# Kernel tuning notes

Hardware: AMD Instinct MI355X
Metric: run time of the kernel (lower is better)

The kernel has to match this reference:

```python
import jax, jax.numpy as jnp
import numpy as np

B, C_IN, N = 4, 128, 4096
E = 131072           # nnz edges in the sparse adjacency
C_OUT = 128          # module out_channels
C_CONV = C_OUT - 1   # add_counts=True steals one channel for degree counts


def setup_inputs() -> dict:
    key = jax.random.key(0)
    kx, ki, kj, kw, kb = jax.random.split(key, 5)
    x = jax.random.normal(kx, (B, C_IN, N), dtype=jnp.float32)
    # edge list (i, j) for each nonzero of the sparse adjacency
    idx_i = jax.random.randint(ki, (E,), 0, N)
    idx_j = jax.random.randint(kj, (E,), 0, N)
    # Conv1d(in=C_IN, out=C_CONV, kernel_size=2, stride=2) weights
    W = jax.random.normal(kw, (C_CONV, C_IN, 2), dtype=jnp.float32) * 0.05
    b = jax.random.normal(kb, (C_CONV,), dtype=jnp.float32) * 0.05
    return {"x": x, "W": W, "b": b, "idx_i": idx_i, "idx_j": idx_j}


def reference(x, W, b, idx_i, idx_j):
    # _conv: x @ adj_pw.T is a gather of the two endpoints of every edge
    # (adj_pw row 2k selects node idx_i[k], row 2k+1 selects node idx_j[k]).
    # Conv1d(kernel=2, stride=2) then mixes the interleaved endpoint pair:
    #   pair[b,o,e] = sum_c W[o,c,0]*x[b,c,i_e] + W[o,c,1]*x[b,c,j_e] + b[o]
    xi = x[:, :, idx_i]                                   # [B, C, E]
    xj = x[:, :, idx_j]                                   # [B, C, E]
    pair = (jnp.einsum('oc,bce->boe', W[:, :, 0], xi)
            + jnp.einsum('oc,bce->boe', W[:, :, 1], xj)
            + b[None, :, None])                           # [B, C_CONV, E]
    # x @ adj_pw[::2, :] scatter-adds each edge's output to its first endpoint
    n = x.shape[2]
    y = jnp.zeros((x.shape[0], pair.shape[1], n), dtype=x.dtype)
    y = y.at[:, :, idx_i].add(pair)                       # [B, C_CONV, N]
    # adj_sum = adj.to_dense().sum(dim=0): in-degree over columns j
    deg = jnp.zeros((n,), dtype=x.dtype).at[idx_j].add(1.0)
    # normalize: divide by degree clamped to >= 1
    y = y / jnp.where(deg == 0, 1.0, deg)
    # add_counts: append raw degree as an extra channel
    counts = jnp.broadcast_to(deg[None, None, :], (y.shape[0], 1, n))
    return jnp.concatenate([y, counts], axis=1)           # [B, C_OUT, N]
```

## Files before the change

kernel.cpp:

```cpp
#include <hip/hip_runtime.h>
#include <cstdint>
#include <cstddef>

#define BATCH   4
#define CIN     128
#define NN      4096
#define EE      131072
#define CCONV   127
#define NBC     512
#define MAXDEG  128
#define CPAD    16

typedef __attribute__((ext_vector_type(8))) short short8;
typedef __attribute__((ext_vector_type(8))) unsigned short ushort8;
typedef __attribute__((ext_vector_type(4))) float f32x4;

__device__ __forceinline__ unsigned short f2bf(float f) {
    unsigned int u = __float_as_uint(f);
    return (unsigned short)((u + 0x7FFFu + ((u >> 16) & 1u)) >> 16);
}
__device__ __forceinline__ float bf2f(unsigned short h) {
    return __uint_as_float((unsigned int)h << 16);
}

__global__ __launch_bounds__(256) void k_pre(const float* __restrict__ x,
                                             unsigned short* __restrict__ xT,
                                             const float* __restrict__ W,
                                             unsigned short* __restrict__ WTb,
                                             const int* __restrict__ idx_i,
                                             const int* __restrict__ idx_j,
                                             int* __restrict__ cursor,
                                             unsigned short* __restrict__ elist,
                                             int* __restrict__ deg) {
    const int bid = blockIdx.x;
    const int tid = threadIdx.x;
    if (bid < 256) {
        __shared__ float tile[128][65];
        const int b  = bid & 3;
        const int n0 = (bid >> 2) * 64;
        const int rl = tid >> 4;
        const int l4 = (tid & 15) * 4;
        const float* xb = x + (size_t)b * CIN * NN + n0 + l4;
#pragma unroll
        for (int it = 0; it < 8; ++it) {
            const int c = it * 16 + rl;
            const float4 v = *(const float4*)(xb + (size_t)c * NN);
            tile[c][l4 + 0] = v.x;
            tile[c][l4 + 1] = v.y;
            tile[c][l4 + 2] = v.z;
            tile[c][l4 + 3] = v.w;
        }
        __syncthreads();
        const int l = tid & 63;
#pragma unroll
        for (int it = 0; it < 16; ++it) {
            const int n = it * 4 + (tid >> 6);
            ushort2 r;
            r.x = f2bf(tile[2 * l + 0][n]);
            r.y = f2bf(tile[2 * l + 1][n]);
            *(ushort2*)(xT + (size_t)(n0 + n) * NBC + b * CIN + 2 * l) = r;
        }
    } else if (bid < 768) {
        const int e  = (bid - 256) * 256 + tid;
        const int ni = idx_i[e];
        const int nj = idx_j[e];
        const int pos = atomicAdd(&cursor[ni * CPAD], 1);
        elist[(size_t)ni * MAXDEG + pos] = (unsigned short)nj;
        atomicAdd(&deg[nj * CPAD], 1);
    } else {
        const int t = (bid - 768) * 256 + tid;
        const int o = t >> 8;
        const int k = t & 255;
        float v = 0.0f;
        if (o < CCONV) v = W[((size_t)o * CIN + (k & 127)) * 2 + (k >> 7)];
        WTb[t] = f2bf(v);
    }
}

__global__ __launch_bounds__(256) void k_final(const unsigned short* __restrict__ xT,
                                               const unsigned short* __restrict__ WTb,
                                               const float* __restrict__ bias,
                                               const unsigned short* __restrict__ elist,
                                               const int* __restrict__ cnt_i,
                                               const int* __restrict__ deg,
                                               float* __restrict__ out) {
    __shared__ short Af[512 * 8];
    __shared__ float cntf[16], invd[16], degf[16], biasf[128];
    __shared__ int   cnti[16];

    const int tid = threadIdx.x;
    const int b   = blockIdx.y;
    const int n0  = blockIdx.x * 16;

    if (tid < 16) {
        const int c = cnt_i[(n0 + tid) * CPAD];
        const int d = deg[(n0 + tid) * CPAD];
        cnti[tid] = c;
        cntf[tid] = (float)c;
        degf[tid] = (float)d;
        invd[tid] = (d == 0) ? 1.0f : 1.0f / (float)d;
    } else if (tid >= 64 && tid < 192) {
        const int o = tid - 64;
        biasf[o] = (o < CCONV) ? bias[o] : 0.0f;
    }
    __syncthreads();

    const int lane = tid & 63;
    const int w    = tid >> 6;

    {
        const int ns = lane >> 4;
        const int j  = w * 4 + ns;
        const int c0 = (lane & 15) * 8;
        const unsigned short* xb = xT + b * CIN + c0;
        const int dn = cnti[j];
        const unsigned short* erow = elist + (size_t)(n0 + j) * MAXDEG;
        float acc[8] = {0, 0, 0, 0, 0, 0, 0, 0};
        int k = 0;
        for (; k + 8 <= dn; k += 8) {
            const ushort8 i8 = *(const ushort8*)(erow + k);
            ushort8 u[8];
#pragma unroll
            for (int t = 0; t < 8; ++t)
                u[t] = *(const ushort8*)(xb + (size_t)i8[t] * NBC);
#pragma unroll
            for (int t = 0; t < 8; ++t)
#pragma unroll
                for (int q = 0; q < 8; ++q) acc[q] += bf2f(u[t][q]);
        }
        for (; k < dn; ++k) {
            const ushort8 u = *(const ushort8*)(xb + (size_t)erow[k] * NBC);
#pragma unroll
            for (int q = 0; q < 8; ++q) acc[q] += bf2f(u[q]);
        }
        short8 p;
#pragma unroll
        for (int q = 0; q < 8; ++q) p[q] = (short)f2bf(acc[q]);
        const int kt   = 4 + (c0 >> 5);
        const int g    = (c0 >> 3) & 3;
        const int unit = kt * 64 + 16 * g + j;
        *(short8*)&Af[unit * 8] = p;
    }

    {
        const int L  = tid & 63;
        const int kt = tid >> 6;
        const int j  = L & 15;
        const int k0 = kt * 32 + (L >> 4) * 8;
        const short8 a = *(const short8*)(xT + (size_t)(n0 + j) * NBC + b * CIN + k0);
        const float sc = cntf[j];
        short8 p;
#pragma unroll
        for (int q = 0; q < 8; ++q)
            p[q] = (short)f2bf(bf2f((unsigned short)a[q]) * sc);
        *(short8*)&Af[(kt * 64 + L) * 8] = p;
    }
    __syncthreads();

    const int m = lane & 15;
    const int g = lane >> 4;

    f32x4 acc0 = (f32x4){0.0f, 0.0f, 0.0f, 0.0f};
    f32x4 acc1 = (f32x4){0.0f, 0.0f, 0.0f, 0.0f};

    const unsigned short* B0 = WTb + (size_t)(w * 32 + m) * 256;
    const unsigned short* B1 = B0 + 16 * 256;

#pragma unroll
    for (int kt = 0; kt < 8; ++kt) {
        const int k0 = kt * 32 + g * 8;
        const short8 b0 = *(const short8*)(B0 + k0);
        const short8 b1 = *(const short8*)(B1 + k0);
        const short8 a  = *(const short8*)&Af[(kt * 64 + lane) * 8];
        acc0 = __builtin_amdgcn_mfma_f32_16x16x32_bf16(a, b0, acc0, 0, 0, 0);
        acc1 = __builtin_amdgcn_mfma_f32_16x16x32_bf16(a, b1, acc1, 0, 0, 0);
    }

#pragma unroll
    for (int nt = 0; nt < 2; ++nt) {
        const f32x4 a = nt ? acc1 : acc0;
        const int o = w * 32 + nt * 16 + m;
        if (o >= CCONV) continue;
        const float bo = biasf[o];
        float* orow = out + ((size_t)b * 128 + o) * NN + n0;
        const int j0 = g * 4;
        float4 r;
        r.x = (a[0] + cntf[j0 + 0] * bo) * invd[j0 + 0];
        r.y = (a[1] + cntf[j0 + 1] * bo) * invd[j0 + 1];
        r.z = (a[2] + cntf[j0 + 2] * bo) * invd[j0 + 2];
        r.w = (a[3] + cntf[j0 + 3] * bo) * invd[j0 + 3];
        *(float4*)(orow + j0) = r;
    }
    if (tid < 16)
        out[((size_t)b * 128 + CCONV) * NN + n0 + tid] = degf[tid];
}

extern "C" void kernel_launch(void* const* d_in, const int* in_sizes, int n_in,
                              void* d_out, int out_size, void* d_ws, size_t ws_size,
                              hipStream_t stream) {
    const float* x    = (const float*)d_in[0];
    const float* W    = (const float*)d_in[1];
    const float* bias = (const float*)d_in[2];
    const int* idx_i  = (const int*)d_in[3];
    const int* idx_j  = (const int*)d_in[4];
    float* out = (float*)d_out;

    char* ws = (char*)d_ws;
    unsigned short* xT     = (unsigned short*)(ws);
    unsigned short* elist  = (unsigned short*)(ws + 4194304);
    unsigned short* WTb    = (unsigned short*)(ws + 5242880);
    int*            cursor = (int*)(ws + 5308416);
    int*            deg    = (int*)(ws + 5570560);

    hipMemsetAsync(cursor, 0, 524288, stream);

    k_pre<<<896, 256, 0, stream>>>(x, xT, W, WTb, idx_i, idx_j, cursor, elist, deg);
    k_final<<<dim3(NN / 16, BATCH), 256, 0, stream>>>(xT, WTb, bias, elist, cursor, deg, out);
}
```

Before: 101.4 us.

## Switch intermediates to fp16 with packed half accumulation and prefetched gathers

Converts the transposed activations and weights from bf16 to fp16 and accumulates the neighbor gather sum in packed half8 vectors (two accumulators) in place of per-element fp32 adds, then feeds fp16 MFMA. The gather loop is software-pipelined so the next 8 rows and their indices load while the current rows are summed. Nontemporal loads and stores are added for the input read and output write. Summing in fp16 and scaling x by the count in fp16 reduces precision and risks overflow or accuracy loss at high degrees.

```diff
diff --git a/kernel.cpp b/kernel.cpp
--- a/kernel.cpp
+++ b/kernel.cpp
@@ -13,14 +13,12 @@
 
 typedef __attribute__((ext_vector_type(8))) short short8;
 typedef __attribute__((ext_vector_type(8))) unsigned short ushort8;
+typedef __attribute__((ext_vector_type(8))) _Float16 half8;
 typedef __attribute__((ext_vector_type(4))) float f32x4;
 
-__device__ __forceinline__ unsigned short f2bf(float f) {
-    unsigned int u = __float_as_uint(f);
-    return (unsigned short)((u + 0x7FFFu + ((u >> 16) & 1u)) >> 16);
-}
-__device__ __forceinline__ float bf2f(unsigned short h) {
-    return __uint_as_float((unsigned int)h << 16);
+__device__ __forceinline__ unsigned short f2h(float f) {
+    _Float16 h = (_Float16)f;
+    return __builtin_bit_cast(unsigned short, h);
 }
 
 __global__ __launch_bounds__(256) void k_pre(const float* __restrict__ x,
@@ -44,11 +42,11 @@
 #pragma unroll
         for (int it = 0; it < 8; ++it) {
             const int c = it * 16 + rl;
-            const float4 v = *(const float4*)(xb + (size_t)c * NN);
-            tile[c][l4 + 0] = v.x;
-            tile[c][l4 + 1] = v.y;
-            tile[c][l4 + 2] = v.z;
-            tile[c][l4 + 3] = v.w;
+            const f32x4 v = __builtin_nontemporal_load((const f32x4*)(xb + (size_t)c * NN));
+            tile[c][l4 + 0] = v[0];
+            tile[c][l4 + 1] = v[1];
+            tile[c][l4 + 2] = v[2];
+            tile[c][l4 + 3] = v[3];
         }
         __syncthreads();
         const int l = tid & 63;
@@ -56,8 +54,8 @@
         for (int it = 0; it < 16; ++it) {
             const int n = it * 4 + (tid >> 6);
             ushort2 r;
-            r.x = f2bf(tile[2 * l + 0][n]);
-            r.y = f2bf(tile[2 * l + 1][n]);
+            r.x = f2h(tile[2 * l + 0][n]);
+            r.y = f2h(tile[2 * l + 1][n]);
             *(ushort2*)(xT + (size_t)(n0 + n) * NBC + b * CIN + 2 * l) = r;
         }
     } else if (bid < 768) {
@@ -73,7 +71,7 @@
         const int k = t & 255;
         float v = 0.0f;
         if (o < CCONV) v = W[((size_t)o * CIN + (k & 127)) * 2 + (k >> 7)];
-        WTb[t] = f2bf(v);
+        WTb[t] = f2h(v);
     }
 }
 
@@ -84,7 +82,7 @@
                                                const int* __restrict__ cnt_i,
                                                const int* __restrict__ deg,
                                                float* __restrict__ out) {
-    __shared__ short Af[512 * 8];
+    __shared__ __align__(16) short Af[512 * 8];
     __shared__ float cntf[16], invd[16], degf[16], biasf[128];
     __shared__ int   cnti[16];
 
@@ -115,31 +113,43 @@
         const unsigned short* xb = xT + b * CIN + c0;
         const int dn = cnti[j];
         const unsigned short* erow = elist + (size_t)(n0 + j) * MAXDEG;
-        float acc[8] = {0, 0, 0, 0, 0, 0, 0, 0};
+        half8 accA = {0, 0, 0, 0, 0, 0, 0, 0};
+        half8 accB = {0, 0, 0, 0, 0, 0, 0, 0};
         int k = 0;
-        for (; k + 8 <= dn; k += 8) {
-            const ushort8 i8 = *(const ushort8*)(erow + k);
-            ushort8 u[8];
+        if (dn >= 8) {
+            ushort8 idx  = *(const ushort8*)(erow);
+            ushort8 idxn = *(const ushort8*)(erow + 8);
+            half8 u[8];
 #pragma unroll
             for (int t = 0; t < 8; ++t)
-                u[t] = *(const ushort8*)(xb + (size_t)i8[t] * NBC);
-#pragma unroll
-            for (int t = 0; t < 8; ++t)
-#pragma unroll
-                for (int q = 0; q < 8; ++q) acc[q] += bf2f(u[t][q]);
+                u[t] = *(const half8*)(xb + (size_t)idx[t] * NBC);
+            for (k = 8; k + 8 <= dn; k += 8) {
+                half8 un[8];
+#pragma unroll
+                for (int t = 0; t < 8; ++t)
+                    un[t] = *(const half8*)(xb + (size_t)idxn[t] * NBC);
+                idxn = *(const ushort8*)(erow + k + 8);
+#pragma unroll
+                for (int t = 0; t < 8; t += 2) {
+                    accA += u[t];
+                    accB += u[t + 1];
+                }
+#pragma unroll
+                for (int t = 0; t < 8; ++t) u[t] = un[t];
+            }
+#pragma unroll
+            for (int t = 0; t < 8; t += 2) {
+                accA += u[t];
+                accB += u[t + 1];
+            }
         }
-        for (; k < dn; ++k) {
-            const ushort8 u = *(const ushort8*)(xb + (size_t)erow[k] * NBC);
-#pragma unroll
-            for (int q = 0; q < 8; ++q) acc[q] += bf2f(u[q]);
-        }
-        short8 p;
-#pragma unroll
-        for (int q = 0; q < 8; ++q) p[q] = (short)f2bf(acc[q]);
+        for (; k < dn; ++k)
+            accA += *(const half8*)(xb + (size_t)erow[k] * NBC);
+        const half8 s = accA + accB;
         const int kt   = 4 + (c0 >> 5);
         const int g    = (c0 >> 3) & 3;
         const int unit = kt * 64 + 16 * g + j;
-        *(short8*)&Af[unit * 8] = p;
+        *(half8*)&Af[unit * 8] = s;
     }
 
     {
@@ -147,13 +157,10 @@
         const int kt = tid >> 6;
         const int j  = L & 15;
         const int k0 = kt * 32 + (L >> 4) * 8;
-        const short8 a = *(const short8*)(xT + (size_t)(n0 + j) * NBC + b * CIN + k0);
-        const float sc = cntf[j];
-        short8 p;
-#pragma unroll
-        for (int q = 0; q < 8; ++q)
-            p[q] = (short)f2bf(bf2f((unsigned short)a[q]) * sc);
-        *(short8*)&Af[(kt * 64 + L) * 8] = p;
+        const half8 a = *(const half8*)(xT + (size_t)(n0 + j) * NBC + b * CIN + k0);
+        const _Float16 sc = (_Float16)cntf[j];
+        const half8 p = a * sc;
+        *(half8*)&Af[(kt * 64 + L) * 8] = p;
     }
     __syncthreads();
 
@@ -169,11 +176,11 @@
 #pragma unroll
     for (int kt = 0; kt < 8; ++kt) {
         const int k0 = kt * 32 + g * 8;
-        const short8 b0 = *(const short8*)(B0 + k0);
-        const short8 b1 = *(const short8*)(B1 + k0);
-        const short8 a  = *(const short8*)&Af[(kt * 64 + lane) * 8];
-        acc0 = __builtin_amdgcn_mfma_f32_16x16x32_bf16(a, b0, acc0, 0, 0, 0);
-        acc1 = __builtin_amdgcn_mfma_f32_16x16x32_bf16(a, b1, acc1, 0, 0, 0);
+        const half8 b0 = *(const half8*)(B0 + k0);
+        const half8 b1 = *(const half8*)(B1 + k0);
+        const half8 a  = *(const half8*)&Af[(kt * 64 + lane) * 8];
+        acc0 = __builtin_amdgcn_mfma_f32_16x16x32_f16(a, b0, acc0, 0, 0, 0);
+        acc1 = __builtin_amdgcn_mfma_f32_16x16x32_f16(a, b1, acc1, 0, 0, 0);
     }
 
 #pragma unroll
@@ -184,15 +191,16 @@
         const float bo = biasf[o];
         float* orow = out + ((size_t)b * 128 + o) * NN + n0;
         const int j0 = g * 4;
-        float4 r;
-        r.x = (a[0] + cntf[j0 + 0] * bo) * invd[j0 + 0];
-        r.y = (a[1] + cntf[j0 + 1] * bo) * invd[j0 + 1];
-        r.z = (a[2] + cntf[j0 + 2] * bo) * invd[j0 + 2];
-        r.w = (a[3] + cntf[j0 + 3] * bo) * invd[j0 + 3];
-        *(float4*)(orow + j0) = r;
+        f32x4 r;
+        r[0] = (a[0] + cntf[j0 + 0] * bo) * invd[j0 + 0];
+        r[1] = (a[1] + cntf[j0 + 1] * bo) * invd[j0 + 1];
+        r[2] = (a[2] + cntf[j0 + 2] * bo) * invd[j0 + 2];
+        r[3] = (a[3] + cntf[j0 + 3] * bo) * invd[j0 + 3];
+        __builtin_nontemporal_store(r, (f32x4*)(orow + j0));
     }
     if (tid < 16)
-        out[((size_t)b * 128 + CCONV) * NN + n0 + tid] = degf[tid];
+        __builtin_nontemporal_store(degf[tid],
+                                    &out[((size_t)b * 128 + CCONV) * NN + n0 + tid]);
 }
 
 extern "C" void kernel_launch(void* const* d_in, const int* in_sizes, int n_in,
@@ -212,7 +220,7 @@
     int*            cursor = (int*)(ws + 5308416);
     int*            deg    = (int*)(ws + 5570560);
 
-    hipMemsetAsync(cursor, 0, 524288, stream);
+    (void)hipMemsetAsync(cursor, 0, 524288, stream);
 
     k_pre<<<896, 256, 0, stream>>>(x, xT, W, WTb, idx_i, idx_j, cursor, elist, deg);
     k_final<<<dim3(NN / 16, BATCH), 256, 0, stream>>>(xT, WTb, bias, elist, cursor, deg, out);
```

After: 99.95 us. About the same (-1.4%).
